# Optimization experiments

Measured on AMD Instinct MI355X. Metric: run time of the kernel, lower is better.

The kernel has to match this reference:

```python
import jax, jax.numpy as jnp
import numpy as np

EPS = 1e-5


def _gcn_norm(edge_index, num_nodes):
    # PyG GCNConv default: add self-loops, then sym-normalize D^-1/2 A_hat D^-1/2
    row, col = edge_index[0], edge_index[1]
    loop = jnp.arange(num_nodes, dtype=edge_index.dtype)
    row = jnp.concatenate([row, loop])
    col = jnp.concatenate([col, loop])
    ones = jnp.ones(row.shape[0], dtype=jnp.float32)
    deg = jax.ops.segment_sum(ones, col, num_segments=num_nodes)
    dinv = jnp.where(deg > 0, jax.lax.rsqrt(deg), 0.0)
    norm = dinv[row] * dinv[col]
    return row, col, norm


def _layer_norm(x, gamma, beta):
    mu = jnp.mean(x, axis=-1, keepdims=True)
    var = jnp.mean(jnp.square(x - mu), axis=-1, keepdims=True)
    return (x - mu) * jax.lax.rsqrt(var + EPS) * gamma + beta


def setup_inputs() -> dict:
    key = jax.random.key(0)
    N, E, IN, H, L = 50000, 800000, 16, 64, 3
    ks = jax.random.split(key, 8)
    x = jax.random.normal(ks[0], (N, IN), dtype=jnp.float32)
    edge_index = jax.random.randint(ks[1], (2, E), 0, N, dtype=jnp.int64)
    s = 1.0 / np.sqrt(H)
    W_in = jax.random.normal(ks[2], (IN, H), dtype=jnp.float32) / np.sqrt(IN)
    b_in = jnp.zeros((H,), jnp.float32)
    W_conv = jax.random.normal(ks[3], (L, H, H), dtype=jnp.float32) * s
    b_conv = jnp.zeros((L, H), jnp.float32)
    gamma = jnp.ones((L, H), jnp.float32)
    beta = jnp.zeros((L, H), jnp.float32)
    W_out = jax.random.normal(ks[4], (H, 1), dtype=jnp.float32) * s
    b_out = jnp.zeros((1,), jnp.float32)
    return {"x": x, "edge_index": edge_index, "W_in": W_in, "b_in": b_in,
            "W_conv": W_conv, "b_conv": b_conv, "gamma": gamma, "beta": beta,
            "W_out": W_out, "b_out": b_out}


def reference(x, edge_index, W_in, b_in, W_conv, b_conv, gamma, beta, W_out, b_out):
    N = x.shape[0]
    row, col, norm = _gcn_norm(edge_index, N)
    h = jax.nn.relu(x @ W_in + b_in)  # [N, H]
    num_layers = W_conv.shape[0]
    for i in range(num_layers):
        residual = h
        t = h @ W_conv[i]                              # transform
        msg = t[row] * norm[:, None]                   # gather + scale [E+N, H]
        agg = jax.ops.segment_sum(msg, col, num_segments=N) + b_conv[i]
        h = _layer_norm(agg, gamma[i], beta[i])
        h = jax.nn.relu(h)                             # dropout = identity (eval)
        h = h + residual
    out = h @ W_out + b_out                            # [N, 1]
    return out.reshape(-1)
```

## Files before the change

kernel.cpp:

```cpp
#include <hip/hip_runtime.h>

#define EPS 1e-5f
#define CAP 64
#define RS 256
#define BCAP 32

typedef unsigned short ushort_t;
typedef unsigned char u8;
typedef unsigned int u32;
typedef __attribute__((ext_vector_type(2))) float vf2;


__device__ __forceinline__ ushort_t pk_fp8(float a, float b) {
    return (ushort_t)(__builtin_amdgcn_cvt_pk_fp8_f32(a, b, 0, false) & 0xFFFF);
}
__device__ __forceinline__ vf2 unpk_lo(u32 v) {
    return (vf2)__builtin_amdgcn_cvt_pk_f32_fp8((int)v, false);
}
__device__ __forceinline__ vf2 unpk_hi(u32 v) {
    return (vf2)__builtin_amdgcn_cvt_pk_f32_fp8((int)v, true);
}


__global__ void k_p1_mlp(const int* __restrict__ row, const int* __restrict__ col,
                         u8* __restrict__ blkCnt, u32* __restrict__ seg,
                         int e, int nr, int nblk, int mlp4Blocks,
                         const float* __restrict__ x, const float* __restrict__ Win,
                         const float* __restrict__ bin, float2* __restrict__ h2,
                         ushort_t* __restrict__ tsA, ushort_t* __restrict__ tsB,
                         int n) {
    __shared__ u32 lcnt[256];
    if (blockIdx.x < (unsigned)nblk) {
        lcnt[threadIdx.x] = 0;
        __syncthreads();
        int i4 = blockIdx.x * 256 + threadIdx.x;
        int c[4], rw[4], cnt4 = 0;
        if (i4 < (e >> 2)) {
            int4 c4 = ((const int4*)col)[i4];
            int4 r4 = ((const int4*)row)[i4];
            c[0] = c4.x; c[1] = c4.y; c[2] = c4.z; c[3] = c4.w;
            rw[0] = r4.x; rw[1] = r4.y; rw[2] = r4.z; rw[3] = r4.w;
            cnt4 = 4;
        } else {
            for (int j = 0; j < 4; ++j) {
                int i = 4 * i4 + j;
                if (i < e) { c[cnt4] = col[i]; rw[cnt4] = row[i]; ++cnt4; }
            }
        }
        for (int j = 0; j < cnt4; ++j) {
            int r = c[j] >> 8;
            u32 rank = atomicAdd(&lcnt[r], 1u);
            if (rank < BCAP)
                seg[((size_t)r * nblk + blockIdx.x) * BCAP + rank] =
                    ((u32)c[j] << 16) | (u32)rw[j];
        }
        __syncthreads();
        for (int j = threadIdx.x; j < nr; j += 256)
            blkCnt[(size_t)j * nblk + blockIdx.x] = (u8)min(lcnt[j], (u32)BCAP);
        return;
    }
    int b = blockIdx.x - nblk;
    if (b >= mlp4Blocks) {
        if (threadIdx.x < 16) {
            ((u32*)tsA)[(size_t)n * 16 + threadIdx.x] = 0;
            ((u32*)tsB)[(size_t)n * 16 + threadIdx.x] = 0;
        }
        return;
    }
    int wv = threadIdx.x >> 6, lane = threadIdx.x & 63;
    int qtr = lane >> 4, q = lane & 15;
    int node = b * 16 + wv * 4 + qtr;
    bool alive = node < n;
    int nl = alive ? node : 0;
    float xv = x[(size_t)nl * 16 + q];
    float2 bi0 = *(const float2*)(bin + 2 * q);
    float2 bi1 = *(const float2*)(bin + 32 + 2 * q);
    float s0 = bi0.x, s1 = bi0.y, s2 = bi1.x, s3 = bi1.y;
#pragma unroll
    for (int k = 0; k < 16; ++k) {
        float xk = __shfl(xv, k, 16);
        float2 wa = *(const float2*)(Win + k * 64 + 2 * q);
        float2 wb = *(const float2*)(Win + k * 64 + 32 + 2 * q);
        s0 = fmaf(xk, wa.x, s0); s1 = fmaf(xk, wa.y, s1);
        s2 = fmaf(xk, wb.x, s2); s3 = fmaf(xk, wb.y, s3);
    }
    s0 = fmaxf(s0, 0.0f); s1 = fmaxf(s1, 0.0f);
    s2 = fmaxf(s2, 0.0f); s3 = fmaxf(s3, 0.0f);
    if (alive)
        *(float4*)((float*)h2 + (size_t)nl * 64 + 4 * q) =
            make_float4(s0, s2, s1, s3);
}


__global__ void k_p2t(const u8* __restrict__ blkCnt, const u32* __restrict__ seg,
                      ushort_t* __restrict__ bRowF, int* __restrict__ cnt,
                      const float2* __restrict__ h2, const float* __restrict__ W0,
                      ushort_t* __restrict__ tsA, int nblk, int n) {
    __shared__ ushort_t bkt[RS * CAP];
    __shared__ u32 lcnt[RS];
    int r = blockIdx.x;
    u32 fillv = ((u32)n << 16) | (u32)n;
    u32* bw_ = (u32*)bkt;
    for (int j = threadIdx.x; j < RS * CAP / 2; j += blockDim.x) bw_[j] = fillv;
    for (int j = threadIdx.x; j < RS; j += blockDim.x) lcnt[j] = 0;
    __syncthreads();
    for (int b = threadIdx.x; b < nblk; b += blockDim.x) {
        int cb = blkCnt[(size_t)r * nblk + b];
        const u32* s = seg + ((size_t)r * nblk + b) * BCAP;
        for (int j = 0; j < cb; ++j) {
            u32 p = s[j];
            int cl = (p >> 16) & (RS - 1);
            u32 slot = atomicAdd(&lcnt[cl], 1u);
            if (slot < CAP) bkt[(cl << 6) + slot] = (ushort_t)(p & 0xFFFF);
        }
    }
    __syncthreads();
    int nodeBase = r << 8;
    int nNodes = min(RS, n - nodeBase);
    if (nNodes > 0) {
        u32* dst = (u32*)(bRowF + ((size_t)nodeBase << 6));
        const u32* src = (const u32*)bkt;
        for (int j = threadIdx.x; j < nNodes * 32; j += blockDim.x) dst[j] = src[j];
        for (int j = threadIdx.x; j < nNodes; j += blockDim.x)
            cnt[nodeBase + j] = (int)lcnt[j];
    }
    int wv = threadIdx.x >> 6, lane = threadIdx.x & 63;
    float w[64];
#pragma unroll
    for (int j = 0; j < 64; ++j) {
        int k = (j >> 1) + ((j & 1) << 5);
        w[j] = W0[k * 64 + lane];
    }
    int m = lane & 31;
    int lim = min(16, nNodes - wv * 16);
    for (int i = 0; i < lim; ++i) {
        int ln = wv * 16 + i;
        int nu = __builtin_amdgcn_readfirstlane(nodeBase + ln);
        const float4* yr4 = (const float4*)(h2 + (size_t)nu * 32);
        float a0 = 0.f, a1 = 0.f, a2 = 0.f, a3 = 0.f;
#pragma unroll
        for (int j4 = 0; j4 < 16; ++j4) {
            float4 y = yr4[j4];
            a0 = fmaf(y.x, w[4 * j4 + 0], a0);
            a1 = fmaf(y.y, w[4 * j4 + 1], a1);
            a2 = fmaf(y.z, w[4 * j4 + 2], a2);
            a3 = fmaf(y.w, w[4 * j4 + 3], a3);
        }
        float dv = rsqrtf((float)(lcnt[ln] + 1));
        float t = ((a0 + a1) + (a2 + a3)) * dv;
        float other = __shfl_xor(t, 32);
        if (lane < 32) tsA[(size_t)nu * 32 + m] = pk_fp8(t, other);
    }
}


__global__ __launch_bounds__(256, 4)
void k_gather_f(const int* __restrict__ cnt, const ushort_t* __restrict__ bRow,
                const ushort_t* __restrict__ tsi,
                const float* __restrict__ bc, const float* __restrict__ gm,
                const float* __restrict__ bt, float2* __restrict__ h2, int n,
                const float* __restrict__ Wn, ushort_t* __restrict__ tso,
                const float* __restrict__ Wout, const float* __restrict__ bout,
                float* __restrict__ out, int last) {
    __shared__ float ysm[4][4][64];
    int wv = threadIdx.x >> 6, lane = threadIdx.x & 63;
    int qtr = lane >> 4, q = lane & 15;
    int node = blockIdx.x * 16 + wv * 4 + qtr;
    bool alive = node < n;
    int nl = alive ? node : 0;

    int deg = cnt[nl];
    float dvv = rsqrtf((float)(deg + 1));
    int gneed = alive ? ((min(deg, CAP) + 7) >> 3) : 0;
    int g1 = max(gneed, __shfl_xor(gneed, 16));
    int gmax = __builtin_amdgcn_readfirstlane(max(g1, __shfl_xor(g1, 32)));
    gmax = max(gmax, 1);

    const char* tsb = (const char*)tsi;
    u32 qoff = (u32)q << 2;
    u32 selfw = *(const u32*)(tsb + (((u32)nl << 6) | qoff));
    float4 hv = *(const float4*)((const float*)h2 + (size_t)nl * 64 + 4 * q);
    const uint4* bq = (const uint4*)(bRow + ((size_t)nl << 6));

    vf2 a0 = {0.f, 0.f}, a1 = {0.f, 0.f};
    uint4 bw = bq[0];
    u32 v0 = *(const u32*)(tsb + (((bw.x & 0xFFFFu) << 6) | qoff));
    u32 v1 = *(const u32*)(tsb + (((bw.x >> 16) << 6) | qoff));
    u32 v2 = *(const u32*)(tsb + (((bw.y & 0xFFFFu) << 6) | qoff));
    u32 v3 = *(const u32*)(tsb + (((bw.y >> 16) << 6) | qoff));
    u32 v4 = *(const u32*)(tsb + (((bw.z & 0xFFFFu) << 6) | qoff));
    u32 v5 = *(const u32*)(tsb + (((bw.z >> 16) << 6) | qoff));
    u32 v6 = *(const u32*)(tsb + (((bw.w & 0xFFFFu) << 6) | qoff));
    u32 v7 = *(const u32*)(tsb + (((bw.w >> 16) << 6) | qoff));
    for (int g = 0; g + 1 < gmax; ++g) {
        uint4 bwn = bq[min(g + 1, 7)];
        u32 w0 = *(const u32*)(tsb + (((bwn.x & 0xFFFFu) << 6) | qoff));
        u32 w1 = *(const u32*)(tsb + (((bwn.x >> 16) << 6) | qoff));
        u32 w2 = *(const u32*)(tsb + (((bwn.y & 0xFFFFu) << 6) | qoff));
        u32 w3 = *(const u32*)(tsb + (((bwn.y >> 16) << 6) | qoff));
        u32 w4 = *(const u32*)(tsb + (((bwn.z & 0xFFFFu) << 6) | qoff));
        u32 w5 = *(const u32*)(tsb + (((bwn.z >> 16) << 6) | qoff));
        u32 w6 = *(const u32*)(tsb + (((bwn.w & 0xFFFFu) << 6) | qoff));
        u32 w7 = *(const u32*)(tsb + (((bwn.w >> 16) << 6) | qoff));
        a0 += unpk_lo(v0); a1 += unpk_hi(v0);
        a0 += unpk_lo(v1); a1 += unpk_hi(v1);
        a0 += unpk_lo(v2); a1 += unpk_hi(v2);
        a0 += unpk_lo(v3); a1 += unpk_hi(v3);
        a0 += unpk_lo(v4); a1 += unpk_hi(v4);
        a0 += unpk_lo(v5); a1 += unpk_hi(v5);
        a0 += unpk_lo(v6); a1 += unpk_hi(v6);
        a0 += unpk_lo(v7); a1 += unpk_hi(v7);
        v0 = w0; v1 = w1; v2 = w2; v3 = w3;
        v4 = w4; v5 = w5; v6 = w6; v7 = w7;
    }
    a0 += unpk_lo(v0); a1 += unpk_hi(v0);
    a0 += unpk_lo(v1); a1 += unpk_hi(v1);
    a0 += unpk_lo(v2); a1 += unpk_hi(v2);
    a0 += unpk_lo(v3); a1 += unpk_hi(v3);
    a0 += unpk_lo(v4); a1 += unpk_hi(v4);
    a0 += unpk_lo(v5); a1 += unpk_hi(v5);
    a0 += unpk_lo(v6); a1 += unpk_hi(v6);
    a0 += unpk_lo(v7); a1 += unpk_hi(v7);

    vf2 s0 = unpk_lo(selfw), s1 = unpk_hi(selfw);
    float2 bc0 = *(const float2*)(bc + 2 * q);
    float2 bc1 = *(const float2*)(bc + 32 + 2 * q);
    float vx0 = (a0.x + s0.x) * dvv + bc0.x;
    float vx1 = (a1.x + s1.x) * dvv + bc0.y;
    float vy0 = (a0.y + s0.y) * dvv + bc1.x;
    float vy1 = (a1.y + s1.y) * dvv + bc1.y;
    float s = (vx0 + vx1) + (vy0 + vy1);
#pragma unroll
    for (int off = 8; off; off >>= 1) s += __shfl_xor(s, off, 16);
    float mu = s * (1.0f / 64.0f);
    float d0 = vx0 - mu, d1 = vx1 - mu, d2 = vy0 - mu, d3 = vy1 - mu;
    float qq = (d0 * d0 + d1 * d1) + (d2 * d2 + d3 * d3);
#pragma unroll
    for (int off = 8; off; off >>= 1) qq += __shfl_xor(qq, off, 16);
    float inv = rsqrtf(qq * (1.0f / 64.0f) + EPS);
    float2 g0 = *(const float2*)(gm + 2 * q);
    float2 g1v = *(const float2*)(gm + 32 + 2 * q);
    float2 b0 = *(const float2*)(bt + 2 * q);
    float2 b1 = *(const float2*)(bt + 32 + 2 * q);
    float y00 = fmaxf(d0 * inv * g0.x + b0.x, 0.0f) + hv.x;
    float y01 = fmaxf(d1 * inv * g0.y + b0.y, 0.0f) + hv.z;
    float y10 = fmaxf(d2 * inv * g1v.x + b1.x, 0.0f) + hv.y;
    float y11 = fmaxf(d3 * inv * g1v.y + b1.y, 0.0f) + hv.w;

    if (!last) {
        if (alive)
            *(float4*)((float*)h2 + (size_t)nl * 64 + 4 * q) =
                make_float4(y00, y10, y01, y11);
        float* yw = &ysm[wv][qtr][0];
        yw[2 * q] = y00; yw[2 * q + 1] = y01;
        yw[2 * q + 32] = y10; yw[2 * q + 33] = y11;
        __builtin_amdgcn_wave_barrier();
        const float* ya = &ysm[wv][0][0];
        const float* yb = &ysm[wv][1][0];
        const float* yc = &ysm[wv][2][0];
        const float* yd = &ysm[wv][3][0];
        float t0 = 0.f, t1 = 0.f, t2 = 0.f, t3 = 0.f;
#pragma unroll
        for (int k4 = 0; k4 < 16; ++k4) {
            float4 fa = *(const float4*)(ya + 4 * k4);
            float4 fb = *(const float4*)(yb + 4 * k4);
            float4 fc = *(const float4*)(yc + 4 * k4);
            float4 fd = *(const float4*)(yd + 4 * k4);
            float w0 = Wn[(4 * k4 + 0) * 64 + lane];
            float w1 = Wn[(4 * k4 + 1) * 64 + lane];
            float w2 = Wn[(4 * k4 + 2) * 64 + lane];
            float w3 = Wn[(4 * k4 + 3) * 64 + lane];
            t0 = fmaf(fa.x, w0, fmaf(fa.y, w1, fmaf(fa.z, w2, fmaf(fa.w, w3, t0))));
            t1 = fmaf(fb.x, w0, fmaf(fb.y, w1, fmaf(fb.z, w2, fmaf(fb.w, w3, t1))));
            t2 = fmaf(fc.x, w0, fmaf(fc.y, w1, fmaf(fc.z, w2, fmaf(fc.w, w3, t2))));
            t3 = fmaf(fd.x, w0, fmaf(fd.y, w1, fmaf(fd.z, w2, fmaf(fd.w, w3, t3))));
        }
        float dv0 = __shfl(dvv, 0), dv1 = __shfl(dvv, 16);
        float dv2 = __shfl(dvv, 32), dv3 = __shfl(dvv, 48);
        t0 *= dv0; t1 *= dv1; t2 *= dv2; t3 *= dv3;
        float o0 = __shfl_xor(t0, 32), o1 = __shfl_xor(t1, 32);
        float o2 = __shfl_xor(t2, 32), o3 = __shfl_xor(t3, 32);
        if (lane < 32) {
            int nb0 = blockIdx.x * 16 + wv * 4;
            if (nb0 + 0 < n) tso[((size_t)(nb0 + 0) << 5) + lane] = pk_fp8(t0, o0);
            if (nb0 + 1 < n) tso[((size_t)(nb0 + 1) << 5) + lane] = pk_fp8(t1, o1);
            if (nb0 + 2 < n) tso[((size_t)(nb0 + 2) << 5) + lane] = pk_fp8(t2, o2);
            if (nb0 + 3 < n) tso[((size_t)(nb0 + 3) << 5) + lane] = pk_fp8(t3, o3);
        }
    } else {
        float2 w0 = *(const float2*)(Wout + 2 * q);
        float2 w1 = *(const float2*)(Wout + 32 + 2 * q);
        float o = (y00 * w0.x + y01 * w0.y) + (y10 * w1.x + y11 * w1.y);
#pragma unroll
        for (int off = 8; off; off >>= 1) o += __shfl_xor(o, off, 16);
        if (alive && q == 0) out[nl] = o + bout[0];
    }
}

extern "C" void kernel_launch(void* const* d_in, const int* in_sizes, int n_in,
                              void* d_out, int out_size, void* d_ws, size_t ws_size,
                              hipStream_t stream) {
    const float* x     = (const float*)d_in[0];
    const int*   eidx  = (const int*)d_in[1];
    const float* Win   = (const float*)d_in[2];
    const float* bin   = (const float*)d_in[3];
    const float* Wconv = (const float*)d_in[4];
    const float* bconv = (const float*)d_in[5];
    const float* gamma = (const float*)d_in[6];
    const float* beta  = (const float*)d_in[7];
    const float* Wout  = (const float*)d_in[8];
    const float* bout  = (const float*)d_in[9];
    float* out = (float*)d_out;

    const int N = in_sizes[0] / 16;
    const int E = in_sizes[1] / 2;
    const int L = in_sizes[4] / (64 * 64);

    const int* row = eidx;
    const int* col = eidx + E;

    char* ws = (char*)d_ws;
    size_t off = 0;
    auto alloc = [&](size_t bytes) -> void* {
        size_t p = off;
        off += (bytes + 255) & ~(size_t)255;
        return (void*)(ws + p);
    };
    const int NR   = (N + RS - 1) / RS;
    const int NBLK = (E + 1023) / 1024;
    int*      cnt    = (int*)alloc((size_t)(N + 1) * 4);
    ushort_t* bRowF  = (ushort_t*)alloc((size_t)(N + RS) * CAP * 2);
    u8*       blkCnt = (u8*)alloc((size_t)NR * NBLK);
    u32*      seg    = (u32*)alloc((size_t)NR * NBLK * BCAP * 4);
    ushort_t* tsA    = (ushort_t*)alloc((size_t)(N + 1) * 32 * 2);
    ushort_t* tsB    = (ushort_t*)alloc((size_t)(N + 1) * 32 * 2);
    float2*   h2     = (float2*)alloc((size_t)N * 32 * 8);
    (void)ws_size;

    const int BT = 256;
    int gMLP4 = (N + 15) / 16;
    int gG    = (N + 15) / 16;

    k_p1_mlp<<<NBLK + gMLP4 + 1, BT, 0, stream>>>(row, col, blkCnt, seg, E, NR,
                                                  NBLK, gMLP4, x, Win, bin, h2,
                                                  tsA, tsB, N);
    k_p2t<<<NR, 1024, 0, stream>>>(blkCnt, seg, bRowF, cnt, h2, Wconv, tsA, NBLK, N);

    ushort_t* ti = tsA;
    ushort_t* to = tsB;
    for (int l = 0; l < L; ++l) {
        const float* bc = bconv + (size_t)l * 64;
        const float* gmv = gamma + (size_t)l * 64;
        const float* bt = beta + (size_t)l * 64;
        int last = (l == L - 1);
        const float* Wn = Wconv + (size_t)(last ? l : l + 1) * 4096;
        k_gather_f<<<gG, BT, 0, stream>>>(cnt, bRowF, ti, bc, gmv, bt, h2, N,
                                          Wn, to, Wout, bout, out, last);
        ushort_t* tmp = ti; ti = to; to = tmp;
    }
}
```

Baseline: 180.9 us.

## Move input MLP into bucket kernel, shrink row buckets, pre-transpose conv weights

Halves the row-bucket size (RS 256→128, BCAP 16) so the bucketing kernel uses 512-thread blocks and more of them. It moves the input Linear+ReLU from the first kernel into k_p2t, so h2 is produced next to its consumer. The first kernel instead transposes each conv weight into a float4-friendly layout, letting the gather kernel load one float4 of weights per k4 rather than four scalars. It also vectorises the segment reads with uint4 loads. The cost is fewer edge slots per block-bucket (overflow risk at BCAP 16) and an extra sync in k_p2t.

Measured after the change: 204.2 us. 1.13x slower.

```diff
diff --git a/kernel.cpp b/kernel.cpp
--- a/kernel.cpp
+++ b/kernel.cpp
@@ -2,8 +2,8 @@
 
 #define EPS 1e-5f
 #define CAP 64
-#define RS 256
-#define BCAP 32
+#define RS 128
+#define BCAP 16
 
 typedef unsigned short ushort_t;
 typedef unsigned char u8;
@@ -22,16 +22,16 @@
 }
 
 
-__global__ void k_p1_mlp(const int* __restrict__ row, const int* __restrict__ col,
-                         u8* __restrict__ blkCnt, u32* __restrict__ seg,
-                         int e, int nr, int nblk, int mlp4Blocks,
-                         const float* __restrict__ x, const float* __restrict__ Win,
-                         const float* __restrict__ bin, float2* __restrict__ h2,
-                         ushort_t* __restrict__ tsA, ushort_t* __restrict__ tsB,
-                         int n) {
-    __shared__ u32 lcnt[256];
+__global__ void k_p1(const int* __restrict__ row, const int* __restrict__ col,
+                     u8* __restrict__ blkCnt, u32* __restrict__ seg,
+                     int e, int nr, int nblk,
+                     const float* __restrict__ Wconv, float* __restrict__ Wt,
+                     ushort_t* __restrict__ tsA, ushort_t* __restrict__ tsB,
+                     int n, int L) {
+    __shared__ u32 lcnt[512];
     if (blockIdx.x < (unsigned)nblk) {
         lcnt[threadIdx.x] = 0;
+        lcnt[threadIdx.x + 256] = 0;
         __syncthreads();
         int i4 = blockIdx.x * 256 + threadIdx.x;
         int c[4], rw[4], cnt4 = 0;
@@ -48,7 +48,7 @@
             }
         }
         for (int j = 0; j < cnt4; ++j) {
-            int r = c[j] >> 8;
+            int r = c[j] >> 7;
             u32 rank = atomicAdd(&lcnt[r], 1u);
             if (rank < BCAP)
                 seg[((size_t)r * nblk + blockIdx.x) * BCAP + rank] =
@@ -59,43 +59,31 @@
             blkCnt[(size_t)j * nblk + blockIdx.x] = (u8)min(lcnt[j], (u32)BCAP);
         return;
     }
-    int b = blockIdx.x - nblk;
-    if (b >= mlp4Blocks) {
+    int aux = blockIdx.x - nblk;
+    if (aux == 0) {
         if (threadIdx.x < 16) {
             ((u32*)tsA)[(size_t)n * 16 + threadIdx.x] = 0;
             ((u32*)tsB)[(size_t)n * 16 + threadIdx.x] = 0;
         }
         return;
     }
-    int wv = threadIdx.x >> 6, lane = threadIdx.x & 63;
-    int qtr = lane >> 4, q = lane & 15;
-    int node = b * 16 + wv * 4 + qtr;
-    bool alive = node < n;
-    int nl = alive ? node : 0;
-    float xv = x[(size_t)nl * 16 + q];
-    float2 bi0 = *(const float2*)(bin + 2 * q);
-    float2 bi1 = *(const float2*)(bin + 32 + 2 * q);
-    float s0 = bi0.x, s1 = bi0.y, s2 = bi1.x, s3 = bi1.y;
-#pragma unroll
-    for (int k = 0; k < 16; ++k) {
-        float xk = __shfl(xv, k, 16);
-        float2 wa = *(const float2*)(Win + k * 64 + 2 * q);
-        float2 wb = *(const float2*)(Win + k * 64 + 32 + 2 * q);
-        s0 = fmaf(xk, wa.x, s0); s1 = fmaf(xk, wa.y, s1);
-        s2 = fmaf(xk, wb.x, s2); s3 = fmaf(xk, wb.y, s3);
-    }
-    s0 = fmaxf(s0, 0.0f); s1 = fmaxf(s1, 0.0f);
-    s2 = fmaxf(s2, 0.0f); s3 = fmaxf(s3, 0.0f);
-    if (alive)
-        *(float4*)((float*)h2 + (size_t)nl * 64 + 4 * q) =
-            make_float4(s0, s2, s1, s3);
+    if (aux < L) {
+        const float* Wl = Wconv + (size_t)aux * 4096;
+        float* Wtl = Wt + (size_t)aux * 4096;
+        for (int lin = threadIdx.x; lin < 4096; lin += 256) {
+            int k4 = lin >> 8, rem = lin & 255, o = rem >> 2, j = rem & 3;
+            Wtl[lin] = Wl[(4 * k4 + j) * 64 + o];
+        }
+    }
 }
 
 
 __global__ void k_p2t(const u8* __restrict__ blkCnt, const u32* __restrict__ seg,
                       ushort_t* __restrict__ bRowF, int* __restrict__ cnt,
-                      const float2* __restrict__ h2, const float* __restrict__ W0,
-                      ushort_t* __restrict__ tsA, int nblk, int n) {
+                      const float* __restrict__ x, const float* __restrict__ Win,
+                      const float* __restrict__ bin, float2* __restrict__ h2,
+                      const float* __restrict__ W0, ushort_t* __restrict__ tsA,
+                      int nblk, int n) {
     __shared__ ushort_t bkt[RS * CAP];
     __shared__ u32 lcnt[RS];
     int r = blockIdx.x;
@@ -106,18 +94,26 @@
     __syncthreads();
     for (int b = threadIdx.x; b < nblk; b += blockDim.x) {
         int cb = blkCnt[(size_t)r * nblk + b];
-        const u32* s = seg + ((size_t)r * nblk + b) * BCAP;
-        for (int j = 0; j < cb; ++j) {
-            u32 p = s[j];
-            int cl = (p >> 16) & (RS - 1);
-            u32 slot = atomicAdd(&lcnt[cl], 1u);
-            if (slot < CAP) bkt[(cl << 6) + slot] = (ushort_t)(p & 0xFFFF);
+        const uint4* sp4 = (const uint4*)(seg + ((size_t)r * nblk + b) * BCAP);
+        for (int j0 = 0; j0 < cb; j0 += 4) {
+            uint4 sv = sp4[j0 >> 2];
+            u32 pv[4] = {sv.x, sv.y, sv.z, sv.w};
+#pragma unroll
+            for (int j = 0; j < 4; ++j) {
+                if (j0 + j < cb) {
+                    u32 p = pv[j];
+                    int cl = (p >> 16) & (RS - 1);
+                    u32 slot = atomicAdd(&lcnt[cl], 1u);
+                    if (slot < CAP) bkt[(cl << 6) + slot] = (ushort_t)(p & 0xFFFF);
+                }
+            }
         }
     }
     __syncthreads();
-    int nodeBase = r << 8;
+    int nodeBase = r << 7;
     int nNodes = min(RS, n - nodeBase);
-    if (nNodes > 0) {
+    if (nNodes <= 0) return;
+    {
         u32* dst = (u32*)(bRowF + ((size_t)nodeBase << 6));
         const u32* src = (const u32*)bkt;
         for (int j = threadIdx.x; j < nNodes * 32; j += blockDim.x) dst[j] = src[j];
@@ -125,6 +121,32 @@
             cnt[nodeBase + j] = (int)lcnt[j];
     }
     int wv = threadIdx.x >> 6, lane = threadIdx.x & 63;
+    {
+        int qtr = lane >> 4, q = lane & 15;
+        for (int pass = 0; pass < 4; ++pass) {
+            int ln = wv * 16 + pass * 4 + qtr;
+            if (ln < nNodes) {
+                int node = nodeBase + ln;
+                float xv = x[(size_t)node * 16 + q];
+                float2 bi0 = *(const float2*)(bin + 2 * q);
+                float2 bi1 = *(const float2*)(bin + 32 + 2 * q);
+                float s0 = bi0.x, s1 = bi0.y, s2 = bi1.x, s3 = bi1.y;
+#pragma unroll
+                for (int k = 0; k < 16; ++k) {
+                    float xk = __shfl(xv, k, 16);
+                    float2 wa = *(const float2*)(Win + k * 64 + 2 * q);
+                    float2 wb = *(const float2*)(Win + k * 64 + 32 + 2 * q);
+                    s0 = fmaf(xk, wa.x, s0); s1 = fmaf(xk, wa.y, s1);
+                    s2 = fmaf(xk, wb.x, s2); s3 = fmaf(xk, wb.y, s3);
+                }
+                s0 = fmaxf(s0, 0.0f); s1 = fmaxf(s1, 0.0f);
+                s2 = fmaxf(s2, 0.0f); s3 = fmaxf(s3, 0.0f);
+                *(float4*)((float*)h2 + (size_t)node * 64 + 4 * q) =
+                    make_float4(s0, s2, s1, s3);
+            }
+        }
+    }
+    __syncthreads();
     float w[64];
 #pragma unroll
     for (int j = 0; j < 64; ++j) {
@@ -159,7 +181,7 @@
                 const ushort_t* __restrict__ tsi,
                 const float* __restrict__ bc, const float* __restrict__ gm,
                 const float* __restrict__ bt, float2* __restrict__ h2, int n,
-                const float* __restrict__ Wn, ushort_t* __restrict__ tso,
+                const float* __restrict__ Wtn, ushort_t* __restrict__ tso,
                 const float* __restrict__ Wout, const float* __restrict__ bout,
                 float* __restrict__ out, int last) {
     __shared__ float ysm[4][4][64];
@@ -259,6 +281,7 @@
         const float* yb = &ysm[wv][1][0];
         const float* yc = &ysm[wv][2][0];
         const float* yd = &ysm[wv][3][0];
+        const float4* wt4 = (const float4*)Wtn;
         float t0 = 0.f, t1 = 0.f, t2 = 0.f, t3 = 0.f;
 #pragma unroll
         for (int k4 = 0; k4 < 16; ++k4) {
@@ -266,14 +289,11 @@
             float4 fb = *(const float4*)(yb + 4 * k4);
             float4 fc = *(const float4*)(yc + 4 * k4);
             float4 fd = *(const float4*)(yd + 4 * k4);
-            float w0 = Wn[(4 * k4 + 0) * 64 + lane];
-            float w1 = Wn[(4 * k4 + 1) * 64 + lane];
-            float w2 = Wn[(4 * k4 + 2) * 64 + lane];
-            float w3 = Wn[(4 * k4 + 3) * 64 + lane];
-            t0 = fmaf(fa.x, w0, fmaf(fa.y, w1, fmaf(fa.z, w2, fmaf(fa.w, w3, t0))));
-            t1 = fmaf(fb.x, w0, fmaf(fb.y, w1, fmaf(fb.z, w2, fmaf(fb.w, w3, t1))));
-            t2 = fmaf(fc.x, w0, fmaf(fc.y, w1, fmaf(fc.z, w2, fmaf(fc.w, w3, t2))));
-            t3 = fmaf(fd.x, w0, fmaf(fd.y, w1, fmaf(fd.z, w2, fmaf(fd.w, w3, t3))));
+            float4 w4 = wt4[(k4 << 6) + lane];
+            t0 = fmaf(fa.x, w4.x, fmaf(fa.y, w4.y, fmaf(fa.z, w4.z, fmaf(fa.w, w4.w, t0))));
+            t1 = fmaf(fb.x, w4.x, fmaf(fb.y, w4.y, fmaf(fb.z, w4.z, fmaf(fb.w, w4.w, t1))));
+            t2 = fmaf(fc.x, w4.x, fmaf(fc.y, w4.y, fmaf(fc.z, w4.z, fmaf(fc.w, w4.w, t2))));
+            t3 = fmaf(fd.x, w4.x, fmaf(fd.y, w4.y, fmaf(fd.z, w4.z, fmaf(fd.w, w4.w, t3))));
         }
         float dv0 = __shfl(dvv, 0), dv1 = __shfl(dvv, 16);
         float dv2 = __shfl(dvv, 32), dv3 = __shfl(dvv, 48);
@@ -335,16 +355,15 @@
     ushort_t* tsA    = (ushort_t*)alloc((size_t)(N + 1) * 32 * 2);
     ushort_t* tsB    = (ushort_t*)alloc((size_t)(N + 1) * 32 * 2);
     float2*   h2     = (float2*)alloc((size_t)N * 32 * 8);
+    float*    Wt     = (float*)alloc((size_t)L * 4096 * 4);
     (void)ws_size;
 
-    const int BT = 256;
-    int gMLP4 = (N + 15) / 16;
-    int gG    = (N + 15) / 16;
-
-    k_p1_mlp<<<NBLK + gMLP4 + 1, BT, 0, stream>>>(row, col, blkCnt, seg, E, NR,
-                                                  NBLK, gMLP4, x, Win, bin, h2,
-                                                  tsA, tsB, N);
-    k_p2t<<<NR, 1024, 0, stream>>>(blkCnt, seg, bRowF, cnt, h2, Wconv, tsA, NBLK, N);
+    int gG = (N + 15) / 16;
+
+    k_p1<<<NBLK + L, 256, 0, stream>>>(row, col, blkCnt, seg, E, NR, NBLK,
+                                       Wconv, Wt, tsA, tsB, N, L);
+    k_p2t<<<NR, 512, 0, stream>>>(blkCnt, seg, bRowF, cnt, x, Win, bin, h2,
+                                  Wconv, tsA, NBLK, N);
 
     ushort_t* ti = tsA;
     ushort_t* to = tsB;
@@ -353,9 +372,9 @@
         const float* gmv = gamma + (size_t)l * 64;
         const float* bt = beta + (size_t)l * 64;
         int last = (l == L - 1);
-        const float* Wn = Wconv + (size_t)(last ? l : l + 1) * 4096;
-        k_gather_f<<<gG, BT, 0, stream>>>(cnt, bRowF, ti, bc, gmv, bt, h2, N,
-                                          Wn, to, Wout, bout, out, last);
+        const float* Wtn = Wt + (size_t)(last ? 0 : l + 1) * 4096;
+        k_gather_f<<<gG, 256, 0, stream>>>(cnt, bRowF, ti, bc, gmv, bt, h2, N,
+                                           Wtn, to, Wout, bout, out, last);
         ushort_t* tmp = ti; ti = to; to = tmp;
     }
 }
```
